# Performance work log

Measured on AMD Instinct MI355X. Metric: run time of the kernel, lower is better.

## Reference

```python
import jax, jax.numpy as jnp
import numpy as np

EPS = 1e-06


def setup_inputs() -> dict:
    key = jax.random.key(0)
    k1, k2, k3 = jax.random.split(key, 3)
    L, B, H, D = 4096, 4, 8, 64
    Q = jax.random.normal(k1, (L, B, H, D), dtype=jnp.float32)
    K = jax.random.normal(k2, (L, B, H, D), dtype=jnp.float32)
    V = jax.random.normal(k3, (L, B, H, D), dtype=jnp.float32)
    return {"Q": Q, "K": K, "V": V}


def reference(Q, K, V):
    # feature map: elu(x) + 1 (positive features)
    phiQ = jax.nn.elu(Q) + 1.0  # [L, B, H, D]
    phiK = jax.nn.elu(K) + 1.0  # [L, B, H, D]
    # Associative rewrite of sum_k phiK_k (x) V_k : per-(batch,head) KV state [D, Dv]
    kv = jnp.einsum('lbhd,lbhe->bhde', phiK, V)          # [B, H, D, Dv]
    num = jnp.einsum('lbhd,bhde->lbhe', phiQ, kv)        # [L, B, H, Dv]
    ksum = jnp.sum(phiK, axis=0)                          # [B, H, D]
    den = jnp.einsum('lbhd,bhd->lbh', phiQ, ksum)[..., None]  # [L, B, H, 1]
    return num / (den + EPS)
```

## Files before the change

### kernel.cpp

```cpp
#include <hip/hip_runtime.h>
#include <math.h>


#define L_TOT 4096
#define NBH   32
#define ROWSTRIDE 2048
#define KVSZ  4160
#define EPS_  1e-6f

typedef short s16x8 __attribute__((ext_vector_type(8)));
typedef float f32x4 __attribute__((ext_vector_type(4)));

union FragU { unsigned int u[4]; s16x8 s; };

__device__ __forceinline__ float phi_(float x) {
    return x > 0.0f ? x + 1.0f : __expf(x);
}

__device__ __forceinline__ unsigned int bf16rn_(float x) {
    unsigned int u = __float_as_uint(x);
    return (u + 0x7FFFu + ((u >> 16) & 1u)) >> 16;
}

__device__ __forceinline__ s16x8 frag_from_(const unsigned short* p) {
    uint2 a = *(const uint2*)p;
    uint2 b = *(const uint2*)(p + 4);
    FragU f;
    f.u[0] = a.x; f.u[1] = a.y; f.u[2] = b.x; f.u[3] = b.y;
    return f.s;
}

__global__ __launch_bounds__(256) void kv_partial_kernel(
    const float* __restrict__ K, const float* __restrict__ V,
    float* __restrict__ part, int Lc)
{
    __shared__ __align__(16) unsigned short kphi[64][36];
    __shared__ __align__(16) unsigned short vtr [64][36];

    const int tid  = threadIdx.x;
    const int w    = tid >> 6;
    const int lane = tid & 63;
    const int c    = blockIdx.x;
    const int bh   = blockIdx.y;
    const int l0c  = c * Lc;
    const int ntiles = Lc >> 5;

    const int sr = tid >> 4;
    const int sc = (tid & 15) * 4;
    const size_t bh_off = (size_t)bh * 64;

    const int ar = lane & 15;
    const int ag = lane >> 4;

    f32x4 acc[4];
    f32x4 aks = {0.f, 0.f, 0.f, 0.f};
    #pragma unroll
    for (int n = 0; n < 4; ++n) { f32x4 z = {0.f,0.f,0.f,0.f}; acc[n] = z; }

    FragU onesU;
    #pragma unroll
    for (int p = 0; p < 4; ++p) onesU.u[p] = 0x3F803F80u;
    const s16x8 ones = onesU.s;

    size_t gb = (size_t)(l0c + sr) * ROWSTRIDE + bh_off + sc;
    float4 ka = *(const float4*)(K + gb);
    float4 va = *(const float4*)(V + gb);
    float4 kb = *(const float4*)(K + gb + 16 * ROWSTRIDE);
    float4 vb = *(const float4*)(V + gb + 16 * ROWSTRIDE);

    for (int t = 0; t < ntiles; ++t) {
        {
            float kx[4] = {ka.x, ka.y, ka.z, ka.w};
            float vx[4] = {va.x, va.y, va.z, va.w};
            float ky[4] = {kb.x, kb.y, kb.z, kb.w};
            float vy[4] = {vb.x, vb.y, vb.z, vb.w};
            #pragma unroll
            for (int i = 0; i < 4; ++i) {
                kphi[sc + i][sr]      = (unsigned short)bf16rn_(phi_(kx[i]));
                kphi[sc + i][sr + 16] = (unsigned short)bf16rn_(phi_(ky[i]));
                vtr [sc + i][sr]      = (unsigned short)bf16rn_(vx[i]);
                vtr [sc + i][sr + 16] = (unsigned short)bf16rn_(vy[i]);
            }
        }
        __syncthreads();

        if (t + 1 < ntiles) {
            gb = (size_t)(l0c + (t + 1) * 32 + sr) * ROWSTRIDE + bh_off + sc;
            ka = *(const float4*)(K + gb);
            va = *(const float4*)(V + gb);
            kb = *(const float4*)(K + gb + 16 * ROWSTRIDE);
            vb = *(const float4*)(V + gb + 16 * ROWSTRIDE);
        }

        const s16x8 afrag = frag_from_(&kphi[w * 16 + ar][ag * 8]);

        #pragma unroll
        for (int nt = 0; nt < 4; ++nt) {
            const s16x8 bfrag = frag_from_(&vtr[nt * 16 + ar][ag * 8]);
            acc[nt] = __builtin_amdgcn_mfma_f32_16x16x32_bf16(afrag, bfrag, acc[nt], 0, 0, 0);
        }
        aks = __builtin_amdgcn_mfma_f32_16x16x32_bf16(afrag, ones, aks, 0, 0, 0);

        __syncthreads();
    }

    float* pb = part + ((size_t)c * NBH + bh) * KVSZ;
    #pragma unroll
    for (int nt = 0; nt < 4; ++nt) {
        #pragma unroll
        for (int r = 0; r < 4; ++r) {
            const int d_row = w * 16 + (lane >> 4) * 4 + r;
            const int e_col = nt * 16 + (lane & 15);
            pb[d_row * 64 + e_col] = acc[nt][r];
        }
    }
    if ((lane & 15) == 0) {
        #pragma unroll
        for (int r = 0; r < 4; ++r)
            pb[4096 + w * 16 + (lane >> 4) * 4 + r] = aks[r];
    }
}

__global__ __launch_bounds__(256) void kv_reduce_kernel(
    const float* __restrict__ part, float* __restrict__ fin, int nchunk)
{
    const int i = blockIdx.x * 256 + threadIdx.x;
    if (i >= NBH * KVSZ) return;
    const int bh = i / KVSZ;
    const int r  = i - bh * KVSZ;

    float s = 0.f;
    for (int cc = 0; cc < nchunk; ++cc)
        s += part[((size_t)cc * NBH + bh) * KVSZ + r];

    float* fb = fin + (size_t)bh * KVSZ;
    if (r < 4096) {
        fb[(r & 63) * 64 + (r >> 6)] = s;
    } else {
        fb[r] = s;
    }
}

__global__ __launch_bounds__(256) void attn_out_kernel(
    const float* __restrict__ Q, const float* __restrict__ fin,
    float* __restrict__ out)
{
    __shared__ __align__(16) unsigned short khi[80 * 72];
    __shared__ __align__(16) unsigned short klo[80 * 72];

    const int tid  = threadIdx.x;
    const int lane = tid & 63;
    const int w    = tid >> 6;
    const int bh   = blockIdx.x & 31;
    const int tg   = blockIdx.x >> 5;
    const int wt0  = tg * 128 + w * 32;

    const float* __restrict__ fb = fin + (size_t)bh * KVSZ;

    for (int idx = tid; idx < 2080; idx += 256) {
        const int e = idx >> 5;
        const int p = idx & 31;
        const float2 x2 = *(const float2*)(fb + e * 64 + 2 * p);
        unsigned int u0 = __float_as_uint(x2.x), u1 = __float_as_uint(x2.y);
        unsigned int hi = (u1 & 0xFFFF0000u) | (u0 >> 16);
        float r0 = x2.x - __uint_as_float(u0 & 0xFFFF0000u);
        float r1 = x2.y - __uint_as_float(u1 & 0xFFFF0000u);
        unsigned int lo = (bf16rn_(r1) << 16) | bf16rn_(r0);
        ((unsigned int*)(khi + e * 72))[p] = hi;
        ((unsigned int*)(klo + e * 72))[p] = lo;
    }
    for (int idx = tid; idx < 480; idx += 256) {
        const int e = 65 + (idx >> 5);
        const int p = idx & 31;
        ((unsigned int*)(khi + e * 72))[p] = 0u;
        ((unsigned int*)(klo + e * 72))[p] = 0u;
    }

    const int arow = lane & 15;
    const int agrp = lane >> 4;
    s16x8 ahi[2][2], alo[2][2];
    #pragma unroll
    for (int m = 0; m < 2; ++m) {
        #pragma unroll
        for (int kc = 0; kc < 2; ++kc) {
            const float* qp = Q + (size_t)(wt0 + m*16 + arow) * ROWSTRIDE
                                + (size_t)bh * 64 + kc*32 + agrp*8;
            float4 qa = *(const float4*)qp;
            float4 qb = *(const float4*)(qp + 4);
            float x[8] = {qa.x,qa.y,qa.z,qa.w,qb.x,qb.y,qb.z,qb.w};
            FragU fh, fl;
            #pragma unroll
            for (int p = 0; p < 4; ++p) {
                float p0 = phi_(x[2*p]), p1 = phi_(x[2*p+1]);
                unsigned int u0 = __float_as_uint(p0), u1 = __float_as_uint(p1);
                fh.u[p] = (u1 & 0xFFFF0000u) | (u0 >> 16);
                float r0 = p0 - __uint_as_float(u0 & 0xFFFF0000u);
                float r1 = p1 - __uint_as_float(u1 & 0xFFFF0000u);
                fl.u[p] = (bf16rn_(r1) << 16) | bf16rn_(r0);
            }
            ahi[m][kc] = fh.s;
            alo[m][kc] = fl.s;
        }
    }
    __syncthreads();

    f32x4 acc[2][5];
    #pragma unroll
    for (int m = 0; m < 2; ++m) {
        #pragma unroll
        for (int n = 0; n < 5; ++n) { f32x4 z = {0.f,0.f,0.f,0.f}; acc[m][n] = z; }
    }

    #pragma unroll
    for (int nt = 0; nt < 5; ++nt) {
        #pragma unroll
        for (int kc = 0; kc < 2; ++kc) {
            const int off = (nt*16 + arow) * 72 + kc*32 + agrp*8;
            s16x8 bh_ = *(const s16x8*)(khi + off);
            s16x8 bl_ = *(const s16x8*)(klo + off);
            #pragma unroll
            for (int m = 0; m < 2; ++m) {
                acc[m][nt] = __builtin_amdgcn_mfma_f32_16x16x32_bf16(ahi[m][kc], bh_, acc[m][nt], 0, 0, 0);
                acc[m][nt] = __builtin_amdgcn_mfma_f32_16x16x32_bf16(ahi[m][kc], bl_, acc[m][nt], 0, 0, 0);
                acc[m][nt] = __builtin_amdgcn_mfma_f32_16x16x32_bf16(alo[m][kc], bh_, acc[m][nt], 0, 0, 0);
            }
        }
    }

    const int baddr = (lane & 48) << 2;
    float inv[2][4];
    #pragma unroll
    for (int m = 0; m < 2; ++m) {
        #pragma unroll
        for (int r = 0; r < 4; ++r) {
            float dv = __int_as_float(
                __builtin_amdgcn_ds_bpermute(baddr, __float_as_int(acc[m][4][r])));
            inv[m][r] = 1.0f / (dv + EPS_);
        }
    }

    #pragma unroll
    for (int m = 0; m < 2; ++m) {
        #pragma unroll
        for (int r = 0; r < 4; ++r) {
            const int t = wt0 + m*16 + (lane >> 4) * 4 + r;
            float* op = out + (size_t)t * ROWSTRIDE + (size_t)bh * 64 + (lane & 15);
            #pragma unroll
            for (int nt = 0; nt < 4; ++nt)
                op[nt * 16] = acc[m][nt][r] * inv[m][r];
        }
    }
}

extern "C" void kernel_launch(void* const* d_in, const int* in_sizes, int n_in,
                              void* d_out, int out_size, void* d_ws, size_t ws_size,
                              hipStream_t stream) {
    const float* Q = (const float*)d_in[0];
    const float* K = (const float*)d_in[1];
    const float* V = (const float*)d_in[2];
    float* outp = (float*)d_out;
    float* ws   = (float*)d_ws;

    const size_t slab = (size_t)NBH * KVSZ;
    const size_t cap  = ws_size / (slab * sizeof(float));

    int nchunk = 1;
    {
        const int cand[4] = {16, 8, 4, 2};
        for (int i = 0; i < 4; ++i) {
            if (cap >= (size_t)cand[i] + 1) { nchunk = cand[i]; break; }
        }
    }
    const int Lc = L_TOT / nchunk;

    float* fin  = ws;
    float* part = ws + slab;

    hipLaunchKernelGGL(kv_partial_kernel, dim3(nchunk, NBH), dim3(256), 0, stream,
                       K, V, part, Lc);
    {
        const int nb = (NBH * KVSZ + 255) / 256;
        hipLaunchKernelGGL(kv_reduce_kernel, dim3(nb), dim3(256), 0, stream,
                           part, fin, nchunk);
    }
    hipLaunchKernelGGL(attn_out_kernel, dim3(1024), dim3(256), 0, stream,
                       Q, fin, outp);
}
```

Measured before the change: 41.64 us.

## Replace partial-sum reduce kernel with atomicAdd into zeroed KV state

Drops the separate kv_reduce kernel and the partial-state workspace. Each chunk block now adds its KV and ksum contributions straight into the final buffer with float atomics, writing the transposed layout directly. The buffer is zeroed with a memset first. The chunk count rises to a fixed 32 to raise parallelism. In exchange it adds atomic contention (32 adders per element), a memset launch, and a summation order that is no longer deterministic.

```diff
diff --git a/kernel.cpp b/kernel.cpp
--- a/kernel.cpp
+++ b/kernel.cpp
@@ -6,6 +6,7 @@
 #define NBH   32
 #define ROWSTRIDE 2048
 #define KVSZ  4160
+#define NCHUNK 32
 #define EPS_  1e-6f
 
 typedef short s16x8 __attribute__((ext_vector_type(8)));
@@ -32,7 +33,7 @@
 
 __global__ __launch_bounds__(256) void kv_partial_kernel(
     const float* __restrict__ K, const float* __restrict__ V,
-    float* __restrict__ part, int Lc)
+    float* __restrict__ fin, int Lc)
 {
     __shared__ __align__(16) unsigned short kphi[64][36];
     __shared__ __align__(16) unsigned short vtr [64][36];
@@ -104,40 +105,20 @@
         __syncthreads();
     }
 
-    float* pb = part + ((size_t)c * NBH + bh) * KVSZ;
+    float* fb = fin + (size_t)bh * KVSZ;
     #pragma unroll
     for (int nt = 0; nt < 4; ++nt) {
         #pragma unroll
         for (int r = 0; r < 4; ++r) {
             const int d_row = w * 16 + (lane >> 4) * 4 + r;
             const int e_col = nt * 16 + (lane & 15);
-            pb[d_row * 64 + e_col] = acc[nt][r];
+            atomicAdd(&fb[e_col * 64 + d_row], acc[nt][r]);
         }
     }
     if ((lane & 15) == 0) {
         #pragma unroll
         for (int r = 0; r < 4; ++r)
-            pb[4096 + w * 16 + (lane >> 4) * 4 + r] = aks[r];
-    }
-}
-
-__global__ __launch_bounds__(256) void kv_reduce_kernel(
-    const float* __restrict__ part, float* __restrict__ fin, int nchunk)
-{
-    const int i = blockIdx.x * 256 + threadIdx.x;
-    if (i >= NBH * KVSZ) return;
-    const int bh = i / KVSZ;
-    const int r  = i - bh * KVSZ;
-
-    float s = 0.f;
-    for (int cc = 0; cc < nchunk; ++cc)
-        s += part[((size_t)cc * NBH + bh) * KVSZ + r];
-
-    float* fb = fin + (size_t)bh * KVSZ;
-    if (r < 4096) {
-        fb[(r & 63) * 64 + (r >> 6)] = s;
-    } else {
-        fb[r] = s;
+            atomicAdd(&fb[4096 + w * 16 + (lane >> 4) * 4 + r], aks[r]);
     }
 }
 
@@ -259,30 +240,15 @@
     const float* K = (const float*)d_in[1];
     const float* V = (const float*)d_in[2];
     float* outp = (float*)d_out;
-    float* ws   = (float*)d_ws;
-
-    const size_t slab = (size_t)NBH * KVSZ;
-    const size_t cap  = ws_size / (slab * sizeof(float));
-
-    int nchunk = 1;
-    {
-        const int cand[4] = {16, 8, 4, 2};
-        for (int i = 0; i < 4; ++i) {
-            if (cap >= (size_t)cand[i] + 1) { nchunk = cand[i]; break; }
-        }
-    }
-    const int Lc = L_TOT / nchunk;
-
-    float* fin  = ws;
-    float* part = ws + slab;
-
-    hipLaunchKernelGGL(kv_partial_kernel, dim3(nchunk, NBH), dim3(256), 0, stream,
-                       K, V, part, Lc);
-    {
-        const int nb = (NBH * KVSZ + 255) / 256;
-        hipLaunchKernelGGL(kv_reduce_kernel, dim3(nb), dim3(256), 0, stream,
-                           part, fin, nchunk);
-    }
+    float* fin  = (float*)d_ws;
+
+    const size_t slab_bytes = (size_t)NBH * KVSZ * sizeof(float);
+
+    hipMemsetAsync(fin, 0, slab_bytes, stream);
+
+    const int Lc = L_TOT / NCHUNK;
+    hipLaunchKernelGGL(kv_partial_kernel, dim3(NCHUNK, NBH), dim3(256), 0, stream,
+                       K, V, fin, Lc);
     hipLaunchKernelGGL(attn_out_kernel, dim3(1024), dim3(256), 0, stream,
                        Q, fin, outp);
 }
```

Result: slower. 102.4 us (+145.8%).
